# Optimization experiments

Hardware: AMD Instinct MI355X
Metric: run time of the kernel (lower is better)

## Reference

```python
import jax, jax.numpy as jnp
import numpy as np

N2, N1, N0 = 25000, 50000, 100000   # node counts: latent -> mid -> full
E1, E2 = 500000, 1000000            # edges at mid and full levels
C = 128                             # hidden channels (Dec_HC)
EPS = 1e-5


def setup_inputs() -> dict:
    key = jax.random.key(0)
    ks = jax.random.split(key, 10)
    inp = {
        "x": jax.random.normal(ks[0], (N2, C), jnp.float32),
        "res1": jax.random.normal(ks[1], (N1, 1), jnp.float32),
        "res2": jax.random.normal(ks[2], (N0, 1), jnp.float32),
        "ew1": jax.random.uniform(ks[3], (E1,), jnp.float32),
        "ew2": jax.random.uniform(ks[4], (E2,), jnp.float32),
        "W1": jax.random.normal(ks[5], (C, C), jnp.float32) * (1.0 / np.sqrt(C)),
        "b1": jnp.zeros((C,), jnp.float32),
        "W2": jax.random.normal(ks[6], (C, C), jnp.float32) * (1.0 / np.sqrt(C)),
        "b2": jnp.zeros((C,), jnp.float32),
        "g1w": jnp.ones((C,), jnp.float32),
        "g1b": jnp.zeros((C,), jnp.float32),
        "g1a": jnp.ones((C,), jnp.float32),
        "g2w": jnp.ones((C,), jnp.float32),
        "g2b": jnp.zeros((C,), jnp.float32),
        "g2a": jnp.ones((C,), jnp.float32),
        "ei1": jax.random.randint(ks[7], (2, E1), 0, N1, jnp.int32),
        "ei2": jax.random.randint(ks[8], (2, E2), 0, N0, jnp.int32),
        "perm1": jnp.arange(N2, dtype=jnp.int32),  # kept-node indices into N1
        "perm2": jnp.arange(N1, dtype=jnp.int32),  # kept-node indices into N0
    }
    return inp


def unpool(x, perm, n):
    # index_copy of kept nodes + masked mean-fill (zero_unpooling=False)
    up = jnp.zeros((n, x.shape[1]), x.dtype).at[perm].set(x)
    mask = jnp.ones((n,), bool).at[perm].set(False)
    return jnp.where(mask[:, None], x.mean(0), up)


def gcn_conv(h, ei, ew, W, b, n):
    # GCNConv, improved=False: add self-loops w=1, symmetric normalization
    sl = jnp.arange(n, dtype=ei.dtype)
    row = jnp.concatenate([ei[0], sl])
    col = jnp.concatenate([ei[1], sl])
    w = jnp.concatenate([ew, jnp.ones((n,), ew.dtype)])
    deg = jax.ops.segment_sum(w, col, num_segments=n)
    dinv = jnp.where(deg > 0, jax.lax.rsqrt(jnp.maximum(deg, EPS * 0 + 1e-12)), 0.0)
    norm = dinv[row] * w * dinv[col]          # [E+n]
    hW = h @ W                                 # [n, C]
    out = jax.ops.segment_sum(hW[row] * norm[:, None], col, num_segments=n)
    return out + b


def graph_norm(h, gamma, beta, alpha):
    # single graph (batch all zeros): statistics over all nodes
    mean = h.mean(0)
    c = h - alpha * mean
    var = (c * c).mean(0)
    return gamma * c * jax.lax.rsqrt(var + EPS) + beta


def reference(x, res1, res2, ew1, ew2, W1, b1, W2, b2,
              g1w, g1b, g1a, g2w, g2b, g2a, ei1, ei2, perm1, perm2):
    # layer 0: unpool N2 -> N1, UNet residual add, GCN, GraphNorm, act
    up = unpool(x, perm1, N1) + res1[:, -1:]
    h = gcn_conv(up, ei1, ew1, W1, b1, N1)
    h = jax.nn.relu(graph_norm(h, g1w, g1b, g1a))
    # layer 1 (last): unpool N1 -> N0, GCN, GraphNorm, no activation
    up = unpool(h, perm2, N0) + res2[:, -1:]
    h = gcn_conv(up, ei2, ew2, W2, b2, N0)
    h = graph_norm(h, g2w, g2b, g2a)
    return h
```

## Files before the change

kernel.cpp:

```cpp
#include <hip/hip_runtime.h>

#define CH 128
constexpr int cN2 = 25000, cN1 = 50000, cN0 = 100000;
constexpr int cE1 = 500000, cE2 = 1000000;
constexpr float cEPS = 1e-5f;

static inline int cdiv(int a, int b) { return (a + b - 1) / b; }

__global__ __launch_bounds__(256) void colstats_kernel(const float* __restrict__ in, int n,
                                                       float* __restrict__ s1, float* __restrict__ s2) {
    int tid = threadIdx.x;
    int c = tid & 127;
    int h = tid >> 7;
    float a1 = 0.f, a2 = 0.f;
    for (int r = blockIdx.x * 2 + h; r < n; r += gridDim.x * 2) {
        float v = in[(size_t)r * CH + c];
        a1 += v;
        a2 += v * v;
    }
    __shared__ float l1[256], l2[256];
    l1[tid] = a1;
    l2[tid] = a2;
    __syncthreads();
    if (h == 0) {
        a1 += l1[tid + 128];
        a2 += l2[tid + 128];
        unsafeAtomicAdd(&s1[c], a1);
        unsafeAtomicAdd(&s2[c], a2);
    }
}

__global__ __launch_bounds__(256) void fill_inv_kernel(int* __restrict__ inv, int n) {
    int i = blockIdx.x * 256 + threadIdx.x;
    if (i < n) inv[i] = -1;
}

__global__ __launch_bounds__(256) void scatter_inv_kernel(const int* __restrict__ perm, int* __restrict__ inv, int m) {
    int i = blockIdx.x * 256 + threadIdx.x;
    if (i < m) inv[perm[i]] = i;
}

__global__ __launch_bounds__(256) void unpool_kernel(const float* __restrict__ src, const int* __restrict__ inv,
                                                     const float* __restrict__ colsum, float inv_cnt,
                                                     const float* __restrict__ res, float* __restrict__ out, int n) {
    int idx = blockIdx.x * 256 + threadIdx.x;
    if (idx >= n * 32) return;
    int j = idx >> 5;
    int c4 = (idx & 31) * 4;
    int iv = inv[j];
    float4 v;
    if (iv >= 0) {
        v = *(const float4*)&src[(size_t)iv * CH + c4];
    } else {
        v.x = colsum[c4 + 0] * inv_cnt;
        v.y = colsum[c4 + 1] * inv_cnt;
        v.z = colsum[c4 + 2] * inv_cnt;
        v.w = colsum[c4 + 3] * inv_cnt;
    }
    float rv = res[j];
    v.x += rv; v.y += rv; v.z += rv; v.w += rv;
    *(float4*)&out[(size_t)j * CH + c4] = v;
}

__global__ __launch_bounds__(256) void edge_deg_hist_kernel(const int* __restrict__ col, const float* __restrict__ ew,
                                                            float* __restrict__ deg, int* __restrict__ hist, int E) {
    int e = blockIdx.x * 256 + threadIdx.x;
    if (e < E) {
        int c = col[e];
        unsafeAtomicAdd(&deg[c], ew[e]);
        atomicAdd(&hist[c], 1);
    }
}

__global__ __launch_bounds__(256) void dinv_kernel(float* __restrict__ deg, int n) {
    int i = blockIdx.x * 256 + threadIdx.x;
    if (i < n) deg[i] = rsqrtf(deg[i] + 1.0f);
}

constexpr int SCAN_ITEMS = 1024;

__global__ __launch_bounds__(256) void scan_reduce_kernel(const int* __restrict__ cnt, int* __restrict__ bsum, int n) {
    __shared__ int lds[256];
    int base = blockIdx.x * SCAN_ITEMS;
    int sum = 0;
    for (int i = threadIdx.x; i < SCAN_ITEMS; i += 256) {
        int idx = base + i;
        sum += (idx < n) ? cnt[idx] : 0;
    }
    lds[threadIdx.x] = sum;
    __syncthreads();
    for (int ofs = 128; ofs > 0; ofs >>= 1) {
        if (threadIdx.x < ofs) lds[threadIdx.x] += lds[threadIdx.x + ofs];
        __syncthreads();
    }
    if (threadIdx.x == 0) bsum[blockIdx.x] = lds[0];
}

__global__ __launch_bounds__(1024) void scan_blocksums_kernel(int* __restrict__ bsum, int nb) {
    __shared__ int lds[1024];
    int tid = threadIdx.x;
    int v = (tid < nb) ? bsum[tid] : 0;
    lds[tid] = v;
    __syncthreads();
    for (int ofs = 1; ofs < 1024; ofs <<= 1) {
        int t = (tid >= ofs) ? lds[tid - ofs] : 0;
        __syncthreads();
        lds[tid] += t;
        __syncthreads();
    }
    if (tid < nb) bsum[tid] = lds[tid] - v;
}

__global__ __launch_bounds__(256) void scan_apply_kernel(const int* __restrict__ cnt, const int* __restrict__ bsum,
                                                         int* __restrict__ off, int* __restrict__ cursor, int n) {
    __shared__ int lds[256];
    int tid = threadIdx.x;
    int idx0 = blockIdx.x * SCAN_ITEMS + tid * 4;
    int v[4];
#pragma unroll
    for (int j = 0; j < 4; ++j) {
        int idx = idx0 + j;
        v[j] = (idx < n) ? cnt[idx] : 0;
    }
    int tsum = v[0] + v[1] + v[2] + v[3];
    lds[tid] = tsum;
    __syncthreads();
    for (int ofs = 1; ofs < 256; ofs <<= 1) {
        int t = (tid >= ofs) ? lds[tid - ofs] : 0;
        __syncthreads();
        lds[tid] += t;
        __syncthreads();
    }
    int run = bsum[blockIdx.x] + lds[tid] - tsum;
#pragma unroll
    for (int j = 0; j < 4; ++j) {
        int idx = idx0 + j;
        if (idx < n) {
            off[idx] = run;
            cursor[idx] = run;
        }
        run += v[j];
    }
    if (blockIdx.x == gridDim.x - 1 && tid == 255) off[n] = run;
}

__global__ __launch_bounds__(256) void csr_scatter_kernel(const int* __restrict__ rows, const int* __restrict__ cols,
                                                          const float* __restrict__ ew, const float* __restrict__ dinv,
                                                          int* __restrict__ cursor, int* __restrict__ csr_row,
                                                          float* __restrict__ csr_val, int E) {
    int e = blockIdx.x * 256 + threadIdx.x;
    if (e >= E) return;
    int r = rows[e];
    int c = cols[e];
    int p = atomicAdd(&cursor[c], 1);
    csr_row[p] = r;
    csr_val[p] = dinv[r] * ew[e] * dinv[c];
}

__global__ __launch_bounds__(256) void gemm128_fused_kernel(const float* __restrict__ A, const float* __restrict__ W,
                                                            const float* __restrict__ dinv, const float* __restrict__ bias,
                                                            float* __restrict__ hW, float* __restrict__ outinit, int n) {
    __shared__ float Ws[CH * CH];
    __shared__ float As[32 * CH];
    int tid = threadIdx.x;
    for (int i = tid * 4; i < CH * CH; i += 256 * 4)
        *(float4*)&Ws[i] = *(const float4*)&W[i];
    int rowbase = blockIdx.x * 32;
    for (int i = tid; i < 32 * 32; i += 256) {
        int r = i >> 5, c4 = (i & 31) * 4;
        int gr = min(rowbase + r, n - 1);
        *(float4*)&As[r * CH + c4] = *(const float4*)&A[(size_t)gr * CH + c4];
    }
    __syncthreads();

    int rg = (tid >> 5) * 4;
    int cc = (tid & 31) * 4;
    float acc[4][4] = {};
#pragma unroll 2
    for (int k = 0; k < CH; k += 4) {
        float4 a[4];
#pragma unroll
        for (int r = 0; r < 4; ++r) a[r] = *(const float4*)&As[(rg + r) * CH + k];
#pragma unroll
        for (int s = 0; s < 4; ++s) {
            float4 wv = *(const float4*)&Ws[(k + s) * CH + cc];
#pragma unroll
            for (int r = 0; r < 4; ++r) {
                float as = (s == 0) ? a[r].x : (s == 1) ? a[r].y : (s == 2) ? a[r].z : a[r].w;
                acc[r][0] += as * wv.x;
                acc[r][1] += as * wv.y;
                acc[r][2] += as * wv.z;
                acc[r][3] += as * wv.w;
            }
        }
    }
#pragma unroll
    for (int r = 0; r < 4; ++r) {
        int gr = rowbase + rg + r;
        if (gr < n) {
            float4 v = make_float4(acc[r][0], acc[r][1], acc[r][2], acc[r][3]);
            *(float4*)&hW[(size_t)gr * CH + cc] = v;
            float d = dinv[gr];
            float s = d * d;
            float4 o;
            o.x = v.x * s + bias[cc + 0];
            o.y = v.y * s + bias[cc + 1];
            o.z = v.z * s + bias[cc + 2];
            o.w = v.w * s + bias[cc + 3];
            *(float4*)&outinit[(size_t)gr * CH + cc] = o;
        }
    }
}

__global__ __launch_bounds__(256) void gather_kernel(const float* __restrict__ hW, const int* __restrict__ off,
                                                     const int* __restrict__ csr_row, const float* __restrict__ csr_val,
                                                     float* __restrict__ out, int n) {
    int lane = threadIdx.x & 63;
    int node = blockIdx.x * 4 + (threadIdx.x >> 6);
    if (node >= n) return;
    int s = off[node], e = off[node + 1];
    float ax = 0.f, ay = 0.f;
    int i = s;
    for (; i + 1 < e; i += 2) {
        int r0 = csr_row[i], r1 = csr_row[i + 1];
        float v0 = csr_val[i], v1 = csr_val[i + 1];
        float2 h0 = *(const float2*)&hW[(size_t)r0 * CH + lane * 2];
        float2 h1 = *(const float2*)&hW[(size_t)r1 * CH + lane * 2];
        ax += v0 * h0.x + v1 * h1.x;
        ay += v0 * h0.y + v1 * h1.y;
    }
    if (i < e) {
        int r0 = csr_row[i];
        float v0 = csr_val[i];
        float2 h0 = *(const float2*)&hW[(size_t)r0 * CH + lane * 2];
        ax += v0 * h0.x;
        ay += v0 * h0.y;
    }
    float2 o = *(float2*)&out[(size_t)node * CH + lane * 2];
    o.x += ax;
    o.y += ay;
    *(float2*)&out[(size_t)node * CH + lane * 2] = o;
}

__global__ __launch_bounds__(256) void norm_kernel(float* __restrict__ h, const float* __restrict__ s1,
                                                   const float* __restrict__ s2, const float* __restrict__ gw,
                                                   const float* __restrict__ gb, const float* __restrict__ ga,
                                                   float inv_n, int n, int do_relu) {
    int idx = blockIdx.x * 256 + threadIdx.x;
    if (idx >= n * 32) return;
    int j = idx >> 5;
    int c4 = (idx & 31) * 4;
    float4 v = *(const float4*)&h[(size_t)j * CH + c4];
    float vv[4] = {v.x, v.y, v.z, v.w};
    float o[4];
#pragma unroll
    for (int i = 0; i < 4; ++i) {
        int c = c4 + i;
        float m = s1[c] * inv_n;
        float msq = s2[c] * inv_n;
        float a = ga[c];
        float var = msq + m * m * (a * a - 2.f * a);
        float r = rsqrtf(var + cEPS);
        float cv = vv[i] - a * m;
        float ov = gw[c] * cv * r + gb[c];
        if (do_relu) ov = fmaxf(ov, 0.f);
        o[i] = ov;
    }
    *(float4*)&h[(size_t)j * CH + c4] = make_float4(o[0], o[1], o[2], o[3]);
}

extern "C" void kernel_launch(void* const* d_in, const int* in_sizes, int n_in,
                              void* d_out, int out_size, void* d_ws, size_t ws_size,
                              hipStream_t stream) {
    const float* x    = (const float*)d_in[0];
    const float* res1 = (const float*)d_in[1];
    const float* res2 = (const float*)d_in[2];
    const float* ew1  = (const float*)d_in[3];
    const float* ew2  = (const float*)d_in[4];
    const float* W1   = (const float*)d_in[5];
    const float* b1   = (const float*)d_in[6];
    const float* W2   = (const float*)d_in[7];
    const float* b2   = (const float*)d_in[8];
    const float* g1w  = (const float*)d_in[9];
    const float* g1b  = (const float*)d_in[10];
    const float* g1a  = (const float*)d_in[11];
    const float* g2w  = (const float*)d_in[12];
    const float* g2b  = (const float*)d_in[13];
    const float* g2a  = (const float*)d_in[14];
    const int* ei1    = (const int*)d_in[15];
    const int* ei2    = (const int*)d_in[16];
    const int* perm1  = (const int*)d_in[17];
    const int* perm2  = (const int*)d_in[18];
    float* out = (float*)d_out;

    size_t NC0 = (size_t)cN0 * CH;
    size_t NC1 = (size_t)cN1 * CH;
    float* ws_f  = (float*)d_ws;
    float* upbuf = ws_f;
    float* hW1   = ws_f + NC0;
    float* h1    = ws_f + NC0 + NC1;
    float* hW2   = ws_f + NC0;
    float* deg   = ws_f + 2 * NC0;
    float* stats = deg + cN0;
    int*   inv   = (int*)(stats + 1024);
    int*   hist  = inv + cN0;
    int*   off   = hist + cN0;
    int*   csr_row = off + cN0 + 1;
    float* csr_val = (float*)(csr_row + cE2);
    int*   bsum  = (int*)(csr_val + cE2);

    float* s1x = stats + 0;   float* s2x = stats + 128;
    float* s1a = stats + 256; float* s2a = stats + 384;
    float* sh1 = stats + 512; float* sh2 = stats + 640;
    float* s1b = stats + 768; float* s2b = stats + 896;

    hipMemsetAsync(stats, 0, 1024 * sizeof(float), stream);

    int nb1 = cdiv(cN1, SCAN_ITEMS), nb0 = cdiv(cN0, SCAN_ITEMS);

    colstats_kernel<<<512, 256, 0, stream>>>(x, cN2, s1x, s2x);
    fill_inv_kernel<<<cdiv(cN1, 256), 256, 0, stream>>>(inv, cN1);
    scatter_inv_kernel<<<cdiv(cN2, 256), 256, 0, stream>>>(perm1, inv, cN2);
    unpool_kernel<<<cdiv(cN1 * 32, 256), 256, 0, stream>>>(x, inv, s1x, 1.f / cN2, res1, upbuf, cN1);

    hipMemsetAsync(deg, 0, (size_t)cN1 * sizeof(float), stream);
    hipMemsetAsync(hist, 0, (size_t)cN1 * sizeof(int), stream);
    edge_deg_hist_kernel<<<cdiv(cE1, 256), 256, 0, stream>>>(ei1 + cE1, ew1, deg, hist, cE1);
    dinv_kernel<<<cdiv(cN1, 256), 256, 0, stream>>>(deg, cN1);

    scan_reduce_kernel<<<nb1, 256, 0, stream>>>(hist, bsum, cN1);
    scan_blocksums_kernel<<<1, 1024, 0, stream>>>(bsum, nb1);
    scan_apply_kernel<<<nb1, 256, 0, stream>>>(hist, bsum, off, hist, cN1);
    csr_scatter_kernel<<<cdiv(cE1, 256), 256, 0, stream>>>(ei1, ei1 + cE1, ew1, deg, hist, csr_row, csr_val, cE1);

    gemm128_fused_kernel<<<cdiv(cN1, 32), 256, 0, stream>>>(upbuf, W1, deg, b1, hW1, h1, cN1);
    gather_kernel<<<cdiv(cN1, 4), 256, 0, stream>>>(hW1, off, csr_row, csr_val, h1, cN1);

    colstats_kernel<<<512, 256, 0, stream>>>(h1, cN1, s1a, s2a);
    norm_kernel<<<cdiv(cN1 * 32, 256), 256, 0, stream>>>(h1, s1a, s2a, g1w, g1b, g1a, 1.f / cN1, cN1, 1);
    colstats_kernel<<<512, 256, 0, stream>>>(h1, cN1, sh1, sh2);

    fill_inv_kernel<<<cdiv(cN0, 256), 256, 0, stream>>>(inv, cN0);
    scatter_inv_kernel<<<cdiv(cN1, 256), 256, 0, stream>>>(perm2, inv, cN1);
    unpool_kernel<<<cdiv(cN0 * 32, 256), 256, 0, stream>>>(h1, inv, sh1, 1.f / cN1, res2, upbuf, cN0);

    hipMemsetAsync(deg, 0, (size_t)cN0 * sizeof(float), stream);
    hipMemsetAsync(hist, 0, (size_t)cN0 * sizeof(int), stream);
    edge_deg_hist_kernel<<<cdiv(cE2, 256), 256, 0, stream>>>(ei2 + cE2, ew2, deg, hist, cE2);
    dinv_kernel<<<cdiv(cN0, 256), 256, 0, stream>>>(deg, cN0);

    scan_reduce_kernel<<<nb0, 256, 0, stream>>>(hist, bsum, cN0);
    scan_blocksums_kernel<<<1, 1024, 0, stream>>>(bsum, nb0);
    scan_apply_kernel<<<nb0, 256, 0, stream>>>(hist, bsum, off, hist, cN0);
    csr_scatter_kernel<<<cdiv(cE2, 256), 256, 0, stream>>>(ei2, ei2 + cE2, ew2, deg, hist, csr_row, csr_val, cE2);

    gemm128_fused_kernel<<<cdiv(cN0, 32), 256, 0, stream>>>(upbuf, W2, deg, b2, hW2, out, cN0);
    gather_kernel<<<cdiv(cN0, 4), 256, 0, stream>>>(hW2, off, csr_row, csr_val, out, cN0);

    colstats_kernel<<<512, 256, 0, stream>>>(out, cN0, s1b, s2b);
    norm_kernel<<<cdiv(cN0 * 32, 256), 256, 0, stream>>>(out, s1b, s2b, g2w, g2b, g2a, 1.f / cN0, cN0, 0);
}
```

Measured before the change: 791.1 us.

## Compute degree from CSR and pack row/weight pairs, normalize in gather

```diff
diff --git a/kernel.cpp b/kernel.cpp
--- a/kernel.cpp
+++ b/kernel.cpp
@@ -62,19 +62,9 @@
     *(float4*)&out[(size_t)j * CH + c4] = v;
 }
 
-__global__ __launch_bounds__(256) void edge_deg_hist_kernel(const int* __restrict__ col, const float* __restrict__ ew,
-                                                            float* __restrict__ deg, int* __restrict__ hist, int E) {
+__global__ __launch_bounds__(256) void edge_hist_kernel(const int* __restrict__ col, int* __restrict__ hist, int E) {
     int e = blockIdx.x * 256 + threadIdx.x;
-    if (e < E) {
-        int c = col[e];
-        unsafeAtomicAdd(&deg[c], ew[e]);
-        atomicAdd(&hist[c], 1);
-    }
-}
-
-__global__ __launch_bounds__(256) void dinv_kernel(float* __restrict__ deg, int n) {
-    int i = blockIdx.x * 256 + threadIdx.x;
-    if (i < n) deg[i] = rsqrtf(deg[i] + 1.0f);
+    if (e < E) atomicAdd(&hist[col[e]], 1);
 }
 
 constexpr int SCAN_ITEMS = 1024;
@@ -145,16 +135,24 @@
 }
 
 __global__ __launch_bounds__(256) void csr_scatter_kernel(const int* __restrict__ rows, const int* __restrict__ cols,
-                                                          const float* __restrict__ ew, const float* __restrict__ dinv,
-                                                          int* __restrict__ cursor, int* __restrict__ csr_row,
-                                                          float* __restrict__ csr_val, int E) {
+                                                          const float* __restrict__ ew,
+                                                          int* __restrict__ cursor, int2* __restrict__ csr_pair, int E) {
     int e = blockIdx.x * 256 + threadIdx.x;
     if (e >= E) return;
     int r = rows[e];
     int c = cols[e];
     int p = atomicAdd(&cursor[c], 1);
-    csr_row[p] = r;
-    csr_val[p] = dinv[r] * ew[e] * dinv[c];
+    csr_pair[p] = make_int2(r, __float_as_int(ew[e]));
+}
+
+__global__ __launch_bounds__(256) void deg_dinv_kernel(const int* __restrict__ off, const int2* __restrict__ csr_pair,
+                                                       float* __restrict__ dinv, int n) {
+    int i = blockIdx.x * 256 + threadIdx.x;
+    if (i >= n) return;
+    int s = off[i], e = off[i + 1];
+    float d = 1.0f;
+    for (int p = s; p < e; ++p) d += __int_as_float(csr_pair[p].y);
+    dinv[i] = rsqrtf(d);
 }
 
 __global__ __launch_bounds__(256) void gemm128_fused_kernel(const float* __restrict__ A, const float* __restrict__ W,
@@ -213,7 +211,7 @@
 }
 
 __global__ __launch_bounds__(256) void gather_kernel(const float* __restrict__ hW, const int* __restrict__ off,
-                                                     const int* __restrict__ csr_row, const float* __restrict__ csr_val,
+                                                     const int2* __restrict__ csr_pair, const float* __restrict__ dinv,
                                                      float* __restrict__ out, int n) {
     int lane = threadIdx.x & 63;
     int node = blockIdx.x * 4 + (threadIdx.x >> 6);
@@ -222,23 +220,25 @@
     float ax = 0.f, ay = 0.f;
     int i = s;
     for (; i + 1 < e; i += 2) {
-        int r0 = csr_row[i], r1 = csr_row[i + 1];
-        float v0 = csr_val[i], v1 = csr_val[i + 1];
-        float2 h0 = *(const float2*)&hW[(size_t)r0 * CH + lane * 2];
-        float2 h1 = *(const float2*)&hW[(size_t)r1 * CH + lane * 2];
+        int2 p0 = csr_pair[i], p1 = csr_pair[i + 1];
+        float v0 = __int_as_float(p0.y) * dinv[p0.x];
+        float v1 = __int_as_float(p1.y) * dinv[p1.x];
+        float2 h0 = *(const float2*)&hW[(size_t)p0.x * CH + lane * 2];
+        float2 h1 = *(const float2*)&hW[(size_t)p1.x * CH + lane * 2];
         ax += v0 * h0.x + v1 * h1.x;
         ay += v0 * h0.y + v1 * h1.y;
     }
     if (i < e) {
-        int r0 = csr_row[i];
-        float v0 = csr_val[i];
-        float2 h0 = *(const float2*)&hW[(size_t)r0 * CH + lane * 2];
+        int2 p0 = csr_pair[i];
+        float v0 = __int_as_float(p0.y) * dinv[p0.x];
+        float2 h0 = *(const float2*)&hW[(size_t)p0.x * CH + lane * 2];
         ax += v0 * h0.x;
         ay += v0 * h0.y;
     }
+    float dc = dinv[node];
     float2 o = *(float2*)&out[(size_t)node * CH + lane * 2];
-    o.x += ax;
-    o.y += ay;
+    o.x += dc * ax;
+    o.y += dc * ay;
     *(float2*)&out[(size_t)node * CH + lane * 2] = o;
 }
 
@@ -300,14 +300,13 @@
     float* hW1   = ws_f + NC0;
     float* h1    = ws_f + NC0 + NC1;
     float* hW2   = ws_f + NC0;
-    float* deg   = ws_f + 2 * NC0;
-    float* stats = deg + cN0;
+    float* dinv  = ws_f + 2 * NC0;
+    float* stats = dinv + cN0;
     int*   inv   = (int*)(stats + 1024);
     int*   hist  = inv + cN0;
     int*   off   = hist + cN0;
-    int*   csr_row = off + cN0 + 1;
-    float* csr_val = (float*)(csr_row + cE2);
-    int*   bsum  = (int*)(csr_val + cE2);
+    int2*  csr_pair = (int2*)(off + cN0 + 1);
+    int*   bsum  = (int*)(csr_pair + cE2);
 
     float* s1x = stats + 0;   float* s2x = stats + 128;
     float* s1a = stats + 256; float* s2a = stats + 384;
@@ -323,18 +322,16 @@
     scatter_inv_kernel<<<cdiv(cN2, 256), 256, 0, stream>>>(perm1, inv, cN2);
     unpool_kernel<<<cdiv(cN1 * 32, 256), 256, 0, stream>>>(x, inv, s1x, 1.f / cN2, res1, upbuf, cN1);
 
-    hipMemsetAsync(deg, 0, (size_t)cN1 * sizeof(float), stream);
     hipMemsetAsync(hist, 0, (size_t)cN1 * sizeof(int), stream);
-    edge_deg_hist_kernel<<<cdiv(cE1, 256), 256, 0, stream>>>(ei1 + cE1, ew1, deg, hist, cE1);
-    dinv_kernel<<<cdiv(cN1, 256), 256, 0, stream>>>(deg, cN1);
-
+    edge_hist_kernel<<<cdiv(cE1, 256), 256, 0, stream>>>(ei1 + cE1, hist, cE1);
     scan_reduce_kernel<<<nb1, 256, 0, stream>>>(hist, bsum, cN1);
     scan_blocksums_kernel<<<1, 1024, 0, stream>>>(bsum, nb1);
     scan_apply_kernel<<<nb1, 256, 0, stream>>>(hist, bsum, off, hist, cN1);
-    csr_scatter_kernel<<<cdiv(cE1, 256), 256, 0, stream>>>(ei1, ei1 + cE1, ew1, deg, hist, csr_row, csr_val, cE1);
-
-    gemm128_fused_kernel<<<cdiv(cN1, 32), 256, 0, stream>>>(upbuf, W1, deg, b1, hW1, h1, cN1);
-    gather_kernel<<<cdiv(cN1, 4), 256, 0, stream>>>(hW1, off, csr_row, csr_val, h1, cN1);
+    csr_scatter_kernel<<<cdiv(cE1, 256), 256, 0, stream>>>(ei1, ei1 + cE1, ew1, hist, csr_pair, cE1);
+    deg_dinv_kernel<<<cdiv(cN1, 256), 256, 0, stream>>>(off, csr_pair, dinv, cN1);
+
+    gemm128_fused_kernel<<<cdiv(cN1, 32), 256, 0, stream>>>(upbuf, W1, dinv, b1, hW1, h1, cN1);
+    gather_kernel<<<cdiv(cN1, 4), 256, 0, stream>>>(hW1, off, csr_pair, dinv, h1, cN1);
 
     colstats_kernel<<<512, 256, 0, stream>>>(h1, cN1, s1a, s2a);
     norm_kernel<<<cdiv(cN1 * 32, 256), 256, 0, stream>>>(h1, s1a, s2a, g1w, g1b, g1a, 1.f / cN1, cN1, 1);
@@ -344,18 +341,16 @@
     scatter_inv_kernel<<<cdiv(cN1, 256), 256, 0, stream>>>(perm2, inv, cN1);
     unpool_kernel<<<cdiv(cN0 * 32, 256), 256, 0, stream>>>(h1, inv, sh1, 1.f / cN1, res2, upbuf, cN0);
 
-    hipMemsetAsync(deg, 0, (size_t)cN0 * sizeof(float), stream);
     hipMemsetAsync(hist, 0, (size_t)cN0 * sizeof(int), stream);
-    edge_deg_hist_kernel<<<cdiv(cE2, 256), 256, 0, stream>>>(ei2 + cE2, ew2, deg, hist, cE2);
-    dinv_kernel<<<cdiv(cN0, 256), 256, 0, stream>>>(deg, cN0);
-
+    edge_hist_kernel<<<cdiv(cE2, 256), 256, 0, stream>>>(ei2 + cE2, hist, cE2);
     scan_reduce_kernel<<<nb0, 256, 0, stream>>>(hist, bsum, cN0);
     scan_blocksums_kernel<<<1, 1024, 0, stream>>>(bsum, nb0);
     scan_apply_kernel<<<nb0, 256, 0, stream>>>(hist, bsum, off, hist, cN0);
-    csr_scatter_kernel<<<cdiv(cE2, 256), 256, 0, stream>>>(ei2, ei2 + cE2, ew2, deg, hist, csr_row, csr_val, cE2);
-
-    gemm128_fused_kernel<<<cdiv(cN0, 32), 256, 0, stream>>>(upbuf, W2, deg, b2, hW2, out, cN0);
-    gather_kernel<<<cdiv(cN0, 4), 256, 0, stream>>>(hW2, off, csr_row, csr_val, out, cN0);
+    csr_scatter_kernel<<<cdiv(cE2, 256), 256, 0, stream>>>(ei2, ei2 + cE2, ew2, hist, csr_pair, cE2);
+    deg_dinv_kernel<<<cdiv(cN0, 256), 256, 0, stream>>>(off, csr_pair, dinv, cN0);
+
+    gemm128_fused_kernel<<<cdiv(cN0, 32), 256, 0, stream>>>(upbuf, W2, dinv, b2, hW2, out, cN0);
+    gather_kernel<<<cdiv(cN0, 4), 256, 0, stream>>>(hW2, off, csr_pair, dinv, out, cN0);
 
     colstats_kernel<<<512, 256, 0, stream>>>(out, cN0, s1b, s2b);
     norm_kernel<<<cdiv(cN0 * 32, 256), 256, 0, stream>>>(out, s1b, s2b, g2w, g2b, g2a, 1.f / cN0, cN0, 0);
```

Result: faster. 736.0 us (-7.0%).
